# Optimization experiments

Hardware: AMD Instinct MI355X
Metric: run time of the kernel (lower is better)

## Reference

```python
import jax, jax.numpy as jnp
import numpy as np

PH = PW = 5  # roi_size
EPS = 1e-5


def _conv1x1(x, w, b):
    # x: (B,Cin,H,W), w: (Cout,Cin)
    return jnp.einsum('bchw,oc->bohw', x, w) + b[None, :, None, None]


def _resize_ac(x, oh, ow):
    # F.interpolate bilinear, align_corners=True. x: (B,C,H,W)
    B, C, H, W = x.shape
    ys = jnp.linspace(0.0, H - 1.0, oh)
    xs = jnp.linspace(0.0, W - 1.0, ow)
    y0 = jnp.floor(ys).astype(jnp.int32); y1 = jnp.minimum(y0 + 1, H - 1)
    x0 = jnp.floor(xs).astype(jnp.int32); x1 = jnp.minimum(x0 + 1, W - 1)
    ly = (ys - y0)[:, None]; lx = (xs - x0)[None, :]
    v00 = x[:, :, y0[:, None], x0[None, :]]
    v01 = x[:, :, y0[:, None], x1[None, :]]
    v10 = x[:, :, y1[:, None], x0[None, :]]
    v11 = x[:, :, y1[:, None], x1[None, :]]
    return v00 * (1 - ly) * (1 - lx) + v01 * (1 - ly) * lx + v10 * ly * (1 - lx) + v11 * ly * lx


def _roi_align_one(feat, box):
    # torchvision RoIAlign, spatial_scale=1, sampling_ratio=1, aligned=False
    # feat: (C,H,W), box: (x1,y1,x2,y2)
    C, H, W = feat.shape
    bx1, by1, bx2, by2 = box[0], box[1], box[2], box[3]
    rw = jnp.maximum(bx2 - bx1, 1.0)
    rh = jnp.maximum(by2 - by1, 1.0)
    xs = bx1 + (jnp.arange(PW, dtype=feat.dtype) + 0.5) * (rw / PW)
    ys = by1 + (jnp.arange(PH, dtype=feat.dtype) + 0.5) * (rh / PH)
    yg = jnp.broadcast_to(ys[:, None], (PH, PW))
    xg = jnp.broadcast_to(xs[None, :], (PH, PW))
    valid = (yg >= -1.0) & (yg <= H) & (xg >= -1.0) & (xg <= W)
    y = jnp.clip(yg, 0.0, H - 1.0); x = jnp.clip(xg, 0.0, W - 1.0)
    y0 = jnp.floor(y).astype(jnp.int32); x0 = jnp.floor(x).astype(jnp.int32)
    y1i = jnp.minimum(y0 + 1, H - 1); x1i = jnp.minimum(x0 + 1, W - 1)
    ly = y - y0; lx = x - x0
    v = (feat[:, y0, x0] * (1 - ly) * (1 - lx) + feat[:, y0, x1i] * (1 - ly) * lx
         + feat[:, y1i, x0] * ly * (1 - lx) + feat[:, y1i, x1i] * ly * lx)
    return v * valid  # (C,PH,PW)


def _layernorm(x, w, b):
    mu = jnp.mean(x, -1, keepdims=True)
    var = jnp.var(x, -1, keepdims=True)
    return (x - mu) * jax.lax.rsqrt(var + EPS) * w + b


def setup_inputs() -> dict:
    key = jax.random.key(0)
    ks = jax.random.split(key, 16)
    B, G, NB, HF = 8, 8, 16, 28
    x4 = jax.random.normal(ks[0], (B, 1024, 14, 14), jnp.float32)
    x5 = jax.random.normal(ks[1], (B, 2048, 7, 7), jnp.float32)
    bx = jax.random.uniform(ks[2], (B, NB), minval=0.0, maxval=18.0)
    by = jax.random.uniform(ks[3], (B, NB), minval=0.0, maxval=18.0)
    bw = jax.random.uniform(ks[4], (B, NB), minval=3.0, maxval=10.0)
    bh = jax.random.uniform(ks[5], (B, NB), minval=3.0, maxval=10.0)
    boxes = jnp.stack([bx, by, jnp.minimum(bx + bw, 28.0), jnp.minimum(by + bh, 28.0)], -1)
    group = jax.random.randint(ks[6], (B, G, 2), 0, NB, jnp.int32)
    real_in_num = jnp.full((B,), G, jnp.int32)
    label_s = jax.random.randint(ks[7], (B, G), 0, 6, jnp.int64)
    label_s = jnp.where(jnp.arange(G)[None, :] % 3 == 0, -1, label_s)  # exercise both branches
    skeleton = jax.random.normal(ks[8], (B, G, HF, HF), jnp.float32)
    D = 1536 * PH * PW  # 38400
    return {
        'x4': x4, 'x5': x5, 'boxes': boxes, 'skeleton': skeleton,
        'group': group, 'real_in_num': real_in_num, 'label_s': label_s,
        'conv1_w': jax.random.normal(ks[9], (), jnp.float32) * 0.5,
        'conv1_b': jax.random.normal(ks[10], (), jnp.float32) * 0.1,
        'conv2_w': jax.random.normal(ks[11], (512, 1024), jnp.float32) * 0.03,
        'conv2_b': jnp.zeros((512,), jnp.float32),
        'conv3_w': jax.random.normal(ks[12], (1024, 2048), jnp.float32) * 0.02,
        'conv3_b': jnp.zeros((1024,), jnp.float32),
        'norm1_w': jnp.ones((D,), jnp.float32), 'norm1_b': jnp.zeros((D,), jnp.float32),
        'norm2_w': jnp.ones((512,), jnp.float32), 'norm2_b': jnp.zeros((512,), jnp.float32),
        'fc1_w': jax.random.normal(ks[13], (512, D), jnp.float32) * float(np.sqrt(2.0 / D)),
        'fc1_b': jnp.zeros((512,), jnp.float32),
        'fc2_w': jax.random.normal(ks[14], (6, 512), jnp.float32) * float(np.sqrt(2.0 / 512)),
        'fc2_b': jnp.zeros((6,), jnp.float32),
    }


def reference(x4, x5, boxes, skeleton, group, real_in_num, label_s,
              conv1_w, conv1_b, conv2_w, conv2_b, conv3_w, conv3_b,
              norm1_w, norm1_b, norm2_w, norm2_b, fc1_w, fc1_b, fc2_w, fc2_b):
    B, G = skeleton.shape[0], skeleton.shape[1]
    HF, WF = skeleton.shape[2], skeleton.shape[3]
    # backbone heads: 1x1 conv + bilinear upsample (align_corners=True), concat
    f4 = _resize_ac(_conv1x1(x4, conv2_w, conv2_b), HF, WF)   # (B,512,28,28)
    f5 = _resize_ac(_conv1x1(x5, conv3_w, conv3_b), HF, WF)   # (B,1024,28,28)
    app = jnp.concatenate([f4, f5], axis=1)                   # (B,1536,28,28)
    C = app.shape[1]
    # per-person pose gate: 1x1 conv (scalar on single channel) + sigmoid
    gate = jax.nn.sigmoid(skeleton * conv1_w + conv1_b)       # (B,G,28,28)
    gated = gate[:, :, None] * app[:, None]                   # (B,G,C,28,28)
    use_gate = (label_s != -1)[:, :, None, None, None]
    pose_feature = jnp.where(use_gate, gated, app[:, None])   # (B,G,C,28,28)
    # union box of the two interacting people (get_box_tensor)
    bidx = jnp.arange(B)[:, None]
    b1 = boxes[bidx, group[..., 0]]                           # (B,G,4)
    b2 = boxes[bidx, group[..., 1]]
    ub = jnp.stack([jnp.minimum(b1[..., 0], b2[..., 0]), jnp.minimum(b1[..., 1], b2[..., 1]),
                    jnp.maximum(b1[..., 2], b2[..., 2]), jnp.maximum(b1[..., 3], b2[..., 3])], -1)
    # batched RoIAlign over all N = B*G boxes
    feats = pose_feature.reshape(B * G, C, HF, WF)
    rois = jax.vmap(_roi_align_one)(feats, ub.reshape(B * G, 4))  # (N,C,5,5)
    sk = rois.reshape(B * G, -1)                              # (N,38400)
    sk = jax.nn.relu(_layernorm(sk, norm1_w, norm1_b))
    # dropout(p=0.9) is identity in eval mode
    sk = sk @ fc1_w.T + fc1_b
    sk = _layernorm(sk, norm2_w, norm2_b)
    score = sk @ fc2_w.T + fc2_b                              # (N,6)
    return score
```

## Files before the change

kernel.cpp:

```cpp
#include <hip/hip_runtime.h>
#include <math.h>

#define B8   8
#define HW4  196
#define HW5  49
#define HFW  28
#define NPIX 784
#define CAPP 1536
#define D1   38400
#define NR   64

typedef short short8 __attribute__((ext_vector_type(8)));
typedef short short4v __attribute__((ext_vector_type(4)));
typedef float floatx16 __attribute__((ext_vector_type(16)));

__device__ __forceinline__ unsigned short f2bf(float f) {
  unsigned u = __float_as_uint(f);
  u += 0x7FFF + ((u >> 16) & 1);
  return (unsigned short)(u >> 16);
}

struct Params {
  const float *x4, *x5, *boxes, *skel;
  const int *group, *label;
  const float *c1w, *c1b, *w2c, *b2c, *w3c, *b3c;
  const float *n1w, *n1b, *n2w, *n2b, *fw1, *fb1, *fw2, *fb2;
  float* out;
  unsigned short *x4T, *x5T, *sknT, *w2cH, *w3cH;
  float *f4T, *f5T, *tap4w, *tap5w, *descw, *roisP, *stats, *out1;
  int *tap4o, *tap5o, *desco;
};

struct Sh0 { float tile[6432]; };
struct GemmSh {
  unsigned short As[4096];
  unsigned short Bs[4096];
};
struct Sh2 {
  float cw4[16], cw5[16], wgs;
  int co4[16], co5[16];
  float red[8];
};
struct Sh3 { float tile[6424]; };
struct Sh5 { float red[8]; float red2[24]; };

template <bool BHALF>
__device__ __forceinline__ void gemm_unit(
    GemmSh& sh, const unsigned short* __restrict__ A, const void* __restrict__ Bw,
    float* __restrict__ C, int mt, int nt, int k0, int kchunk,
    int K, int N, int Mvalid, bool accum) {
  int t = threadIdx.x;
  int wave = t >> 6, lane = t & 63;
  int wm = wave & 1, wn = wave >> 1;
  const unsigned short* Aptr = A + (size_t)(mt * 64) * K + k0;
  const unsigned short* Bph = (const unsigned short*)Bw + (size_t)(nt * 64) * K + k0;
  const float* Bpf = (const float*)Bw + (size_t)(nt * 64) * K + k0;

  int m0 = t >> 3, ka = (t & 7) * 8, koa = t & 7;
  int n0 = t >> 4, kbo = (t & 15) * 4, kob = (t & 15) >> 1, half = t & 1;

  short8 areg[2];
  short8 bregh[2];
  float4 breg[4];
  floatx16 acc;
#pragma unroll
  for (int i = 0; i < 16; i++) acc[i] = 0.f;
  int nkb = kchunk >> 6;

  auto LOAD = [&](int j) {
    int kof = j * 64;
    areg[0] = *(const short8*)(Aptr + (size_t)m0 * K + kof + ka);
    areg[1] = *(const short8*)(Aptr + (size_t)(m0 + 32) * K + kof + ka);
    if constexpr (BHALF) {
      bregh[0] = *(const short8*)(Bph + (size_t)m0 * K + kof + ka);
      bregh[1] = *(const short8*)(Bph + (size_t)(m0 + 32) * K + kof + ka);
    } else {
#pragma unroll
      for (int i = 0; i < 4; i++)
        breg[i] = *(const float4*)(Bpf + (size_t)(n0 + 16 * i) * K + kof + kbo);
    }
  };
  auto STORE = [&]() {
    *(short8*)&sh.As[koa * 512 + ((m0 ^ koa)) * 8] = areg[0];
    *(short8*)&sh.As[koa * 512 + (((m0 + 32) ^ koa)) * 8] = areg[1];
    if constexpr (BHALF) {
      *(short8*)&sh.Bs[koa * 512 + ((m0 ^ koa)) * 8] = bregh[0];
      *(short8*)&sh.Bs[koa * 512 + (((m0 + 32) ^ koa)) * 8] = bregh[1];
    } else {
#pragma unroll
      for (int i = 0; i < 4; i++) {
        short4v v;
        v[0] = (short)f2bf(breg[i].x); v[1] = (short)f2bf(breg[i].y);
        v[2] = (short)f2bf(breg[i].z); v[3] = (short)f2bf(breg[i].w);
        int n = n0 + 16 * i;
        *(short4v*)&sh.Bs[kob * 512 + ((n ^ kob)) * 8 + half * 4] = v;
      }
    }
  };

  LOAD(0);
  STORE();
  __syncthreads();

  for (int kb = 0; kb < nkb; kb++) {
    bool more = (kb + 1) < nkb;
    if (more) LOAD(kb + 1);
#pragma unroll
    for (int s = 0; s < 4; s++) {
      int ko = 2 * s + (lane >> 5);
      int am = wm * 32 + (lane & 31);
      int bn = wn * 32 + (lane & 31);
      short8 af = *(const short8*)&sh.As[ko * 512 + ((am ^ ko)) * 8];
      short8 bf = *(const short8*)&sh.Bs[ko * 512 + ((bn ^ ko)) * 8];
      acc = __builtin_amdgcn_mfma_f32_32x32x16_bf16(af, bf, acc, 0, 0, 0);
    }
    __syncthreads();
    if (more) {
      STORE();
      __syncthreads();
    }
  }

  int col = nt * 64 + wn * 32 + (lane & 31);
  int rbase = mt * 64 + wm * 32 + 4 * (lane >> 5);
  if (accum) {
#pragma unroll
    for (int reg = 0; reg < 16; reg++) {
      int row = rbase + (reg & 3) + 8 * (reg >> 2);
      if (row < Mvalid) atomicAdd(&C[(size_t)row * N + col], acc[reg]);
    }
  } else {
#pragma unroll
    for (int reg = 0; reg < 16; reg++) {
      int row = rbase + (reg & 3) + 8 * (reg >> 2);
      if (row < Mvalid) C[(size_t)row * N + col] = acc[reg];
    }
  }
}

__device__ __forceinline__ float gate_val(const float* sk, int yy, int xx,
                                          float c1w, float c1b, bool use) {
  if (!use) return 1.f;
  float z = sk[yy * HFW + xx] * c1w + c1b;
  return 1.f / (1.f + expf(-z));
}

__global__ __launch_bounds__(256, 4) void k_phase0(Params p) {
  __shared__ Sh0 sh;
  int bid = blockIdx.x, t = threadIdx.x, gb = gridDim.x;
  int gtid = bid * 256 + t;
  int nth = gb * 256;
  float4 z4 = make_float4(0.f, 0.f, 0.f, 0.f);
  for (int i = gtid; i < 319488; i += nth) ((float4*)p.f4T)[i] = z4;
  for (int i = gtid; i < 8192; i += nth) ((float4*)p.out1)[i] = z4;
  if (gtid < 128) p.stats[gtid] = 0.f;
  for (int i = gtid; i < 131072; i += nth) {
    float4 v = ((const float4*)p.w2c)[i];
    short4v h;
    h[0] = (short)f2bf(v.x); h[1] = (short)f2bf(v.y);
    h[2] = (short)f2bf(v.z); h[3] = (short)f2bf(v.w);
    *(short4v*)&p.w2cH[i * 4] = h;
  }
  for (int i = gtid; i < 524288; i += nth) {
    float4 v = ((const float4*)p.w3c)[i];
    short4v h;
    h[0] = (short)f2bf(v.x); h[1] = (short)f2bf(v.y);
    h[2] = (short)f2bf(v.z); h[3] = (short)f2bf(v.w);
    *(short4v*)&p.w3cH[i * 4] = h;
  }

  for (int u = bid; u < 836; u += gb) {
    __syncthreads();
    if (u < 256) {
      int b = u >> 5, cc = u & 31;
      for (int i = t; i < 32 * HW4; i += 256) {
        int c = i / HW4, hw = i - c * HW4;
        sh.tile[c * 201 + hw] = p.x4[((size_t)(b * 1024 + cc * 32 + c)) * HW4 + hw];
      }
      __syncthreads();
      for (int i = t; i < HW4 * 8; i += 256) {
        int hw = i >> 3, c4 = (i & 7) * 4;
        short4v h;
#pragma unroll
        for (int q = 0; q < 4; q++) h[q] = (short)f2bf(sh.tile[(c4 + q) * 201 + hw]);
        *(short4v*)&p.x4T[((size_t)(b * HW4 + hw)) * 1024 + cc * 32 + c4] = h;
      }
    } else if (u < 768) {
      int u2 = u - 256;
      int b = u2 >> 6, cc = u2 & 63;
      for (int i = t; i < 32 * HW5; i += 256) {
        int c = i / HW5, hw = i - c * HW5;
        sh.tile[c * 51 + hw] = p.x5[((size_t)(b * 2048 + cc * 32 + c)) * HW5 + hw];
      }
      __syncthreads();
      for (int i = t; i < HW5 * 8; i += 256) {
        int hw = i >> 3, c4 = (i & 7) * 4;
        short4v h;
#pragma unroll
        for (int q = 0; q < 4; q++) h[q] = (short)f2bf(sh.tile[(c4 + q) * 51 + hw]);
        *(short4v*)&p.x5T[((size_t)(b * HW5 + hw)) * 2048 + cc * 32 + c4] = h;
      }
    } else if (u < 832) {
      int bg = u - 768;
      if (t < 25) {
        int b = bg >> 3;
        int i1 = p.group[bg * 2 + 0], i2 = p.group[bg * 2 + 1];
        const float* bb1 = p.boxes + (size_t)(b * 16 + i1) * 4;
        const float* bb2 = p.boxes + (size_t)(b * 16 + i2) * 4;
        float ux1 = fminf(bb1[0], bb2[0]);
        float uy1 = fminf(bb1[1], bb2[1]);
        float ux2 = fmaxf(bb1[2], bb2[2]);
        float uy2 = fmaxf(bb1[3], bb2[3]);
        float rw = fmaxf(ux2 - ux1, 1.0f), rh = fmaxf(uy2 - uy1, 1.0f);
        int iy = t / 5, ix = t % 5;
        float sy = uy1 + (iy + 0.5f) * (rh * 0.2f);
        float sx = ux1 + (ix + 0.5f) * (rw * 0.2f);
        float valid = (sy >= -1.0f && sy <= 28.0f && sx >= -1.0f && sx <= 28.0f) ? 1.f : 0.f;
        float y = fminf(fmaxf(sy, 0.f), 27.f);
        float x = fminf(fmaxf(sx, 0.f), 27.f);
        int y0 = (int)floorf(y), x0 = (int)floorf(x);
        int y1 = min(y0 + 1, 27), x1 = min(x0 + 1, 27);
        float ly = y - (float)y0, lx = x - (float)x0;
        bool use = (p.label[bg] != -1);
        float c1w = p.c1w[0], c1b = p.c1b[0];
        const float* sk = p.skel + (size_t)bg * NPIX;
        int idx = (bg * 25 + t) * 4;
        p.descw[idx + 0] = (1.f - ly) * (1.f - lx) * valid * gate_val(sk, y0, x0, c1w, c1b, use);
        p.descw[idx + 1] = (1.f - ly) * lx * valid * gate_val(sk, y0, x1, c1w, c1b, use);
        p.descw[idx + 2] = ly * (1.f - lx) * valid * gate_val(sk, y1, x0, c1w, c1b, use);
        p.descw[idx + 3] = ly * lx * valid * gate_val(sk, y1, x1, c1w, c1b, use);
        p.desco[idx + 0] = y0 * HFW + x0;
        p.desco[idx + 1] = y0 * HFW + x1;
        p.desco[idx + 2] = y1 * HFW + x0;
        p.desco[idx + 3] = y1 * HFW + x1;
      }
    } else {
      int pix = (u - 832) * 196 + t;
      if (t < 196) {
        int y = pix / HFW, x = pix % HFW;
        {
          float sy = y * (13.0f / 27.0f), sx = x * (13.0f / 27.0f);
          int y0 = (int)sy, x0 = (int)sx;
          int y1 = min(y0 + 1, 13), x1 = min(x0 + 1, 13);
          float ly = sy - y0, lx = sx - x0;
          p.tap4o[pix * 4 + 0] = y0 * 14 + x0; p.tap4w[pix * 4 + 0] = (1.f - ly) * (1.f - lx);
          p.tap4o[pix * 4 + 1] = y0 * 14 + x1; p.tap4w[pix * 4 + 1] = (1.f - ly) * lx;
          p.tap4o[pix * 4 + 2] = y1 * 14 + x0; p.tap4w[pix * 4 + 2] = ly * (1.f - lx);
          p.tap4o[pix * 4 + 3] = y1 * 14 + x1; p.tap4w[pix * 4 + 3] = ly * lx;
        }
        {
          float sy = y * (6.0f / 27.0f), sx = x * (6.0f / 27.0f);
          int y0 = (int)sy, x0 = (int)sx;
          int y1 = min(y0 + 1, 6), x1 = min(x0 + 1, 6);
          float ly = sy - y0, lx = sx - x0;
          p.tap5o[pix * 4 + 0] = y0 * 7 + x0; p.tap5w[pix * 4 + 0] = (1.f - ly) * (1.f - lx);
          p.tap5o[pix * 4 + 1] = y0 * 7 + x1; p.tap5w[pix * 4 + 1] = (1.f - ly) * lx;
          p.tap5o[pix * 4 + 2] = y1 * 7 + x0; p.tap5w[pix * 4 + 2] = ly * (1.f - lx);
          p.tap5o[pix * 4 + 3] = y1 * 7 + x1; p.tap5w[pix * 4 + 3] = ly * lx;
        }
      }
    }
  }
}

__global__ __launch_bounds__(256, 4) void k_phase1(Params p) {
  __shared__ GemmSh sh;
  int bid = blockIdx.x, gb = gridDim.x;
  for (int uu = bid; uu < 1696; uu += gb) {
    int u = (uu & 7) * 212 + (uu >> 3);
    __syncthreads();
    if (u < 800) {
      int mt = u % 25, r = u / 25;
      int nt = r & 7, sp = r >> 3;
      gemm_unit<true>(sh, p.x4T, p.w2cH, p.f4T, mt, nt, sp * 256, 256, 1024, 512, 1568, true);
    } else {
      int u2 = u - 800;
      int mt = u2 % 7, r = u2 / 7;
      int nt = r & 15, sp = r >> 4;
      gemm_unit<true>(sh, p.x5T, p.w3cH, p.f5T, mt, nt, sp * 256, 256, 2048, 1024, 392, true);
    }
  }
}

__global__ __launch_bounds__(256, 4) void k_phase2(Params p) {
  __shared__ Sh2 sh;
  int bid = blockIdx.x, t = threadIdx.x, gb = gridDim.x;
  for (int uu = bid; uu < 1600; uu += gb) {
    int u = (uu & 7) * 200 + (uu >> 3);
    __syncthreads();
    int pp = u % 25, bg = u / 25, b = bg >> 3;
    int di = (bg * 25 + pp) * 4;
    if (t < 16) {
      int i = t >> 2, j = t & 3;
      float wg = p.descw[di + i];
      int pix = p.desco[di + i];
      sh.cw4[t] = wg * p.tap4w[pix * 4 + j];
      sh.co4[t] = (b * HW4 + p.tap4o[pix * 4 + j]) * 512;
      sh.cw5[t] = wg * p.tap5w[pix * 4 + j];
      sh.co5[t] = (b * HW5 + p.tap5o[pix * 4 + j]) * 1024;
    }
    if (t == 16) sh.wgs = p.descw[di] + p.descw[di + 1] + p.descw[di + 2] + p.descw[di + 3];
    __syncthreads();
    float w4r[16], w5r[16];
    int o4r[16], o5r[16];
    float wg = sh.wgs;
#pragma unroll
    for (int i = 0; i < 16; i++) {
      w4r[i] = sh.cw4[i]; o4r[i] = sh.co4[i];
      w5r[i] = sh.cw5[i]; o5r[i] = sh.co5[i];
    }
    float ls = 0.f, ls2 = 0.f;
    float* outp = p.roisP + (size_t)(bg * 25 + pp) * CAPP;
    for (int c = t; c < 512; c += 256) {
      float acc = wg * p.b2c[c];
#pragma unroll
      for (int i = 0; i < 16; i++) acc = fmaf(w4r[i], p.f4T[o4r[i] + c], acc);
      outp[c] = acc;
      ls += acc; ls2 = fmaf(acc, acc, ls2);
    }
    for (int c = t; c < 1024; c += 256) {
      float acc = wg * p.b3c[c];
#pragma unroll
      for (int i = 0; i < 16; i++) acc = fmaf(w5r[i], p.f5T[o5r[i] + c], acc);
      outp[512 + c] = acc;
      ls += acc; ls2 = fmaf(acc, acc, ls2);
    }
    for (int off = 32; off; off >>= 1) {
      ls += __shfl_down(ls, off);
      ls2 += __shfl_down(ls2, off);
    }
    int wv = t >> 6;
    if ((t & 63) == 0) { sh.red[wv] = ls; sh.red[4 + wv] = ls2; }
    __syncthreads();
    if (t == 0) {
      atomicAdd(&p.stats[bg * 2 + 0], sh.red[0] + sh.red[1] + sh.red[2] + sh.red[3]);
      atomicAdd(&p.stats[bg * 2 + 1], sh.red[4] + sh.red[5] + sh.red[6] + sh.red[7]);
    }
  }
}

__global__ __launch_bounds__(256, 4) void k_phase3(Params p) {
  __shared__ Sh3 sh;
  int bid = blockIdx.x, t = threadIdx.x, gb = gridDim.x;
  for (int u = bid; u < 384; u += gb) {
    __syncthreads();
    int r = u / 6, ch = u - r * 6;
    int c0 = ch * 256;
    float S = p.stats[r * 2], S2 = p.stats[r * 2 + 1];
    float mu = S * (1.f / D1);
    float var = S2 * (1.f / D1) - mu * mu;
    float rs = rsqrtf(var + 1e-5f);
    const float* rp = p.roisP + (size_t)r * 25 * CAPP + c0;
#pragma unroll
    for (int pp = 0; pp < 25; pp++)
      sh.tile[pp * 257 + t] = rp[(size_t)pp * CAPP + t];
    __syncthreads();
    unsigned short* op = p.sknT + (size_t)r * D1 + c0 * 25;
    const float* wv = p.n1w + c0 * 25;
    const float* bv = p.n1b + c0 * 25;
    for (int j = t; j < 6400; j += 256) {
      unsigned cc = (unsigned)j / 25u;
      unsigned pp = (unsigned)j - cc * 25u;
      float x = sh.tile[pp * 257 + cc];
      float v = fmaf((x - mu) * rs, wv[j], bv[j]);
      op[j] = f2bf(fmaxf(v, 0.f));
    }
  }
}

__global__ __launch_bounds__(256, 4) void k_phase4(Params p) {
  __shared__ GemmSh sh;
  int bid = blockIdx.x, gb = gridDim.x;
  for (int uu = bid; uu < 960; uu += gb) {
    int u = (uu & 7) * 120 + (uu >> 3);
    __syncthreads();
    int nt = u & 7, sp = u >> 3;
    gemm_unit<false>(sh, p.sknT, p.fw1, p.out1, 0, nt, sp * 320, 320, 38400, 512, 64, true);
  }
}

__global__ __launch_bounds__(256, 4) void k_phase5(Params p) {
  __shared__ Sh5 sh;
  int bid = blockIdx.x, t = threadIdx.x, gb = gridDim.x;
  for (int r = bid; r < NR; r += gb) {
    __syncthreads();
    int j1 = t, j2 = t + 256;
    float v1 = p.out1[r * 512 + j1] + p.fb1[j1];
    float v2 = p.out1[r * 512 + j2] + p.fb1[j2];
    float s = v1 + v2, s2 = v1 * v1 + v2 * v2;
    for (int off = 32; off; off >>= 1) {
      s += __shfl_down(s, off);
      s2 += __shfl_down(s2, off);
    }
    int wv = t >> 6;
    if ((t & 63) == 0) { sh.red[wv] = s; sh.red[4 + wv] = s2; }
    __syncthreads();
    float S = sh.red[0] + sh.red[1] + sh.red[2] + sh.red[3];
    float S2 = sh.red[4] + sh.red[5] + sh.red[6] + sh.red[7];
    float mu = S / 512.f;
    float var = S2 / 512.f - mu * mu;
    float rs = rsqrtf(var + 1e-5f);
    float n1v = fmaf((v1 - mu) * rs, p.n2w[j1], p.n2b[j1]);
    float n2v = fmaf((v2 - mu) * rs, p.n2w[j2], p.n2b[j2]);
    float pm[6];
#pragma unroll
    for (int m = 0; m < 6; m++)
      pm[m] = n1v * p.fw2[m * 512 + j1] + n2v * p.fw2[m * 512 + j2];
#pragma unroll
    for (int m = 0; m < 6; m++)
      for (int off = 32; off; off >>= 1) pm[m] += __shfl_down(pm[m], off);
    if ((t & 63) == 0) {
#pragma unroll
      for (int m = 0; m < 6; m++) sh.red2[wv * 6 + m] = pm[m];
    }
    __syncthreads();
    if (t < 6)
      p.out[r * 6 + t] = sh.red2[t] + sh.red2[6 + t] + sh.red2[12 + t] +
                         sh.red2[18 + t] + p.fb2[t];
  }
}

extern "C" void kernel_launch(void* const* d_in, const int* in_sizes, int n_in,
                              void* d_out, int out_size, void* d_ws, size_t ws_size,
                              hipStream_t stream) {
  Params p;
  p.x4    = (const float*)d_in[0];
  p.x5    = (const float*)d_in[1];
  p.boxes = (const float*)d_in[2];
  p.skel  = (const float*)d_in[3];
  p.group = (const int*)d_in[4];
  p.label = (const int*)d_in[6];
  p.c1w   = (const float*)d_in[7];
  p.c1b   = (const float*)d_in[8];
  p.w2c   = (const float*)d_in[9];
  p.b2c   = (const float*)d_in[10];
  p.w3c   = (const float*)d_in[11];
  p.b3c   = (const float*)d_in[12];
  p.n1w   = (const float*)d_in[13];
  p.n1b   = (const float*)d_in[14];
  p.n2w   = (const float*)d_in[15];
  p.n2b   = (const float*)d_in[16];
  p.fw1   = (const float*)d_in[17];
  p.fb1   = (const float*)d_in[18];
  p.fw2   = (const float*)d_in[19];
  p.fb2   = (const float*)d_in[20];
  p.out   = (float*)d_out;

  float* ws = (float*)d_ws;
  p.x4T   = (unsigned short*)ws;
  p.x5T   = (unsigned short*)(ws + 819200);
  p.f4T   = ws + 1277952;
  p.f5T   = ws + 2097152;
  p.tap4w = ws + 2555904;
  p.tap4o = (int*)(ws + 2559040);
  p.tap5w = ws + 2562176;
  p.tap5o = (int*)(ws + 2565312);
  p.descw = ws + 2568448;
  p.desco = (int*)(ws + 2574848);
  p.roisP = ws + 2581248;
  p.stats = ws + 5038848;
  p.sknT  = (unsigned short*)(ws + 5038976);
  p.out1  = ws + 6267776;
  p.w2cH  = (unsigned short*)(ws + 6300544);
  p.w3cH  = (unsigned short*)(ws + 6562688);

  k_phase0<<<836,  256, 0, stream>>>(p);
  k_phase1<<<1696, 256, 0, stream>>>(p);
  k_phase2<<<1600, 256, 0, stream>>>(p);
  k_phase3<<<384,  256, 0, stream>>>(p);
  k_phase4<<<960,  256, 0, stream>>>(p);
  k_phase5<<<64,   256, 0, stream>>>(p);
}
```

Measured before the change: 237.1 us.

## Fuse LayerNorm1+ReLU into phase2 via last-block-done counter

Removes the separate phase3 kernel and performs the first LayerNorm, ReLU and bf16 transpose inside phase2. A per-row atomic counter picks the last of the 25 contributing blocks, and that block reads the completed stats and normalises the whole 38400-element row. This saves one kernel launch and the inter-kernel gap. In exchange, the normalisation for each row runs serially in a single block, reading the ROI data with a strided, uncoalesced pattern and no shared-memory transpose, and the last block waits on fences and atomics.

```diff
diff --git a/kernel.cpp b/kernel.cpp
--- a/kernel.cpp
+++ b/kernel.cpp
@@ -28,7 +28,7 @@
   float* out;
   unsigned short *x4T, *x5T, *sknT, *w2cH, *w3cH;
   float *f4T, *f5T, *tap4w, *tap5w, *descw, *roisP, *stats, *out1;
-  int *tap4o, *tap5o, *desco;
+  int *tap4o, *tap5o, *desco, *cnt;
 };
 
 struct Sh0 { float tile[6432]; };
@@ -40,8 +40,8 @@
   float cw4[16], cw5[16], wgs;
   int co4[16], co5[16];
   float red[8];
+  int lastf;
 };
-struct Sh3 { float tile[6424]; };
 struct Sh5 { float red[8]; float red2[24]; };
 
 template <bool BHALF>
@@ -154,6 +154,7 @@
   for (int i = gtid; i < 319488; i += nth) ((float4*)p.f4T)[i] = z4;
   for (int i = gtid; i < 8192; i += nth) ((float4*)p.out1)[i] = z4;
   if (gtid < 128) p.stats[gtid] = 0.f;
+  if (gtid < 64) p.cnt[gtid] = 0;
   for (int i = gtid; i < 131072; i += nth) {
     float4 v = ((const float4*)p.w2c)[i];
     short4v h;
@@ -335,35 +336,25 @@
     if (t == 0) {
       atomicAdd(&p.stats[bg * 2 + 0], sh.red[0] + sh.red[1] + sh.red[2] + sh.red[3]);
       atomicAdd(&p.stats[bg * 2 + 1], sh.red[4] + sh.red[5] + sh.red[6] + sh.red[7]);
-    }
-  }
-}
-
-__global__ __launch_bounds__(256, 4) void k_phase3(Params p) {
-  __shared__ Sh3 sh;
-  int bid = blockIdx.x, t = threadIdx.x, gb = gridDim.x;
-  for (int u = bid; u < 384; u += gb) {
-    __syncthreads();
-    int r = u / 6, ch = u - r * 6;
-    int c0 = ch * 256;
-    float S = p.stats[r * 2], S2 = p.stats[r * 2 + 1];
-    float mu = S * (1.f / D1);
-    float var = S2 * (1.f / D1) - mu * mu;
-    float rs = rsqrtf(var + 1e-5f);
-    const float* rp = p.roisP + (size_t)r * 25 * CAPP + c0;
-#pragma unroll
-    for (int pp = 0; pp < 25; pp++)
-      sh.tile[pp * 257 + t] = rp[(size_t)pp * CAPP + t];
-    __syncthreads();
-    unsigned short* op = p.sknT + (size_t)r * D1 + c0 * 25;
-    const float* wv = p.n1w + c0 * 25;
-    const float* bv = p.n1b + c0 * 25;
-    for (int j = t; j < 6400; j += 256) {
-      unsigned cc = (unsigned)j / 25u;
-      unsigned pp = (unsigned)j - cc * 25u;
-      float x = sh.tile[pp * 257 + cc];
-      float v = fmaf((x - mu) * rs, wv[j], bv[j]);
-      op[j] = f2bf(fmaxf(v, 0.f));
+      __threadfence();
+      int old = atomicAdd(&p.cnt[bg], 1);
+      sh.lastf = (old == 24) ? 1 : 0;
+    }
+    __syncthreads();
+    if (sh.lastf) {
+      float S = p.stats[bg * 2], S2 = p.stats[bg * 2 + 1];
+      float mu = S * (1.f / D1);
+      float var = S2 * (1.f / D1) - mu * mu;
+      float rs = rsqrtf(var + 1e-5f);
+      const float* rp = p.roisP + (size_t)bg * 25 * CAPP;
+      unsigned short* op = p.sknT + (size_t)bg * D1;
+      for (int k = t; k < D1; k += 256) {
+        unsigned c = (unsigned)k / 25u;
+        unsigned q = (unsigned)k - c * 25u;
+        float x = rp[(size_t)q * CAPP + c];
+        float v = fmaf((x - mu) * rs, p.n1w[k], p.n1b[k]);
+        op[k] = f2bf(fmaxf(v, 0.f));
+      }
     }
   }
 }
@@ -463,11 +454,11 @@
   p.out1  = ws + 6267776;
   p.w2cH  = (unsigned short*)(ws + 6300544);
   p.w3cH  = (unsigned short*)(ws + 6562688);
+  p.cnt   = (int*)(ws + 7611264);
 
   k_phase0<<<836,  256, 0, stream>>>(p);
   k_phase1<<<1696, 256, 0, stream>>>(p);
   k_phase2<<<1600, 256, 0, stream>>>(p);
-  k_phase3<<<384,  256, 0, stream>>>(p);
   k_phase4<<<960,  256, 0, stream>>>(p);
   k_phase5<<<64,   256, 0, stream>>>(p);
 }
```

After: 330.3 us. 1.39x slower.
